# Optimization experiments

Measured on AMD Instinct MI355X. Metric: run time of the kernel, lower is better.

Reference implementation:

```python
import jax, jax.numpy as jnp
import numpy as np

COMMITMENT_COST = 0.25
EPS = 1e-10


def setup_inputs() -> dict:
    key = jax.random.key(0)
    k1, k2 = jax.random.split(key)
    B, C, H, W = 16, 64, 128, 128          # C == embedding_dim
    K, D = 512, 64                          # codebook size, embedding_dim
    inputs = jax.random.normal(k1, (B, C, H, W), dtype=jnp.float32)
    # nn.Embedding init: uniform(-1/K, 1/K)
    embedding = jax.random.uniform(k2, (K, D), dtype=jnp.float32,
                                   minval=-1.0 / K, maxval=1.0 / K)
    return {"inputs": inputs, "embedding": embedding}


def reference(inputs, embedding):
    # NCHW -> NHWC, flatten to tokens [N, D]
    x = jnp.transpose(inputs, (0, 2, 3, 1))
    nhwc_shape = x.shape
    flat = x.reshape(-1, embedding.shape[1])                       # [N, D]

    distances = (jnp.sum(flat * flat, axis=1, keepdims=True)
                 + jnp.sum(embedding * embedding, axis=1)
                 - 2.0 * flat @ embedding.T)
    idx = jnp.argmin(distances, axis=1)                            # [N]

    # one-hot encodings (returned), quantized via direct gather
    encodings = jax.nn.one_hot(idx, embedding.shape[0], dtype=flat.dtype)  # [N, K]
    quantized = embedding[idx].reshape(nhwc_shape)                 # [B,H,W,D]

    e_latent = jnp.mean((jax.lax.stop_gradient(quantized) - x) ** 2)
    q_latent = jnp.mean((quantized - jax.lax.stop_gradient(x)) ** 2)
    loss = q_latent + COMMITMENT_COST * e_latent

    # straight-through estimator
    quantized_st = x + jax.lax.stop_gradient(quantized - x)

    avg_probs = jnp.mean(encodings, axis=0)                        # [K]
    perplexity = jnp.exp(-jnp.sum(avg_probs * jnp.log(avg_probs + EPS)))

    return (loss, jnp.transpose(quantized_st, (0, 3, 1, 2)), perplexity, encodings)
```

## Files before the change

kernel.cpp:

```cpp
#include <hip/hip_runtime.h>
#include <math.h>


#define NTOK    262144
#define KCODES  512
#define DDIM    64
#define CSTRIDE 16384
#define IMG     1048576
#define QOFF    1
#define POFF    16777217
#define EOFF    16777218
#define BK      8192
#define LOSS    8704
#define EBF     12800
#define SUBFLT  32768

typedef short bf16x8 __attribute__((ext_vector_type(8)));
typedef float f32x4  __attribute__((ext_vector_type(4)));

__device__ __forceinline__ unsigned short f2bf(float f) {
    unsigned u = __float_as_uint(f);
    return (unsigned short)((u + 0x7fffu + ((u >> 16) & 1u)) >> 16);
}

__device__ __forceinline__ float np_pairwise_sq64(const float* v) {
    float r[8];
#pragma unroll
    for (int j = 0; j < 8; ++j) r[j] = __fmul_rn(v[j], v[j]);
#pragma unroll
    for (int i = 8; i < 64; i += 8) {
#pragma unroll
        for (int j = 0; j < 8; ++j)
            r[j] = __fadd_rn(r[j], __fmul_rn(v[i + j], v[i + j]));
    }
    float s01 = __fadd_rn(r[0], r[1]);
    float s23 = __fadd_rn(r[2], r[3]);
    float s45 = __fadd_rn(r[4], r[5]);
    float s67 = __fadd_rn(r[6], r[7]);
    return __fadd_rn(__fadd_rn(s01, s23), __fadd_rn(s45, s67));
}

__global__ __launch_bounds__(256) void vq_prep(const float* __restrict__ emb,
                                               float* __restrict__ ws) {
    const int tid = threadIdx.x, blk = blockIdx.x;
    if (blk < 8) {
        unsigned short* ebf = (unsigned short*)(ws + EBF);
#pragma unroll
        for (int ii = 0; ii < 16; ++ii) {
            int t = blk * 4096 + ii * 256 + tid;
            ebf[t] = f2bf(emb[t]);
        }
    } else {
#pragma unroll
        for (int r = 0; r < 2; ++r) {
            const int k = tid * 2 + r;
            const float* e = emb + (size_t)k * DDIM;
            float v[64];
#pragma unroll
            for (int i = 0; i < 64; ++i) v[i] = e[i];
            ws[BK + k] = np_pairwise_sq64(v);
        }
    }
}

__global__ __launch_bounds__(256, 4) void vq_main(const float* __restrict__ in,
                                                  const float* __restrict__ emb,
                                                  float* __restrict__ out,
                                                  float* __restrict__ ws) {
    __shared__ unsigned short xbf[64 * 68];
    __shared__ float          xls[64 * 64];
    __shared__ float          bsh[512];
    __shared__ int            idx_sh[64];
    __shared__ float          red[4];

    const int tid = threadIdx.x, blk = blockIdx.x;
    const int T0 = blk * 64, b = T0 >> 14, hw0 = T0 & 16383;

    const float4* gx = (const float4*)(in + (size_t)b * IMG + hw0);
    float4 g[4];
#pragma unroll
    for (int jj = 0; jj < 4; ++jj) {
        int t = tid + jj * 256;
        g[jj] = gx[(size_t)(t >> 4) * (CSTRIDE / 4) + (t & 15)];
    }
    const float bk0 = ws[BK + tid];
    const float bk1 = ws[BK + 256 + tid];

    f32x4* sub4 = (f32x4*)(out + EOFF + (size_t)blk * SUBFLT);
    const f32x4 z4 = {0.f, 0.f, 0.f, 0.f};
#pragma unroll
    for (int ii = 0; ii < 32; ++ii)
        __builtin_nontemporal_store(z4, sub4 + ii * 256 + tid);

#pragma unroll
    for (int jj = 0; jj < 4; ++jj) {
        int t = tid + jj * 256;
        int c = t >> 4, q4 = (t & 15) * 4;
        *(float4*)(&xls[c * 64 + q4]) = g[jj];
        xbf[(q4 + 0) * 68 + c] = f2bf(g[jj].x);
        xbf[(q4 + 1) * 68 + c] = f2bf(g[jj].y);
        xbf[(q4 + 2) * 68 + c] = f2bf(g[jj].z);
        xbf[(q4 + 3) * 68 + c] = f2bf(g[jj].w);
    }
    bsh[tid]       = bk0;
    bsh[256 + tid] = bk1;
    __syncthreads();

    const int l = tid & 63, w = tid >> 6;
    const int lm = l & 15, lg = l >> 4;

    const bf16x8 a0 = *(const bf16x8*)(xbf + (w * 16 + lm) * 68 + lg * 8);
    const bf16x8 a1 = *(const bf16x8*)(xbf + (w * 16 + lm) * 68 + 32 + lg * 8);

    const unsigned short* ebf = (const unsigned short*)(ws + EBF);
    const unsigned short* ep  = ebf + lm * 64 + lg * 8;

    float dmin[4]; int idx[4];
#pragma unroll
    for (int r = 0; r < 4; ++r) { dmin[r] = 3.402823466e38f; idx[r] = 0; }
    const f32x4 zero = {0.f, 0.f, 0.f, 0.f};

#pragma unroll 4
    for (int nt = 0; nt < 32; ++nt) {
        bf16x8 b0 = *(const bf16x8*)(ep + nt * 1024);
        bf16x8 b1 = *(const bf16x8*)(ep + nt * 1024 + 32);
        f32x4 acc = __builtin_amdgcn_mfma_f32_16x16x32_bf16(a0, b0, zero, 0, 0, 0);
        acc       = __builtin_amdgcn_mfma_f32_16x16x32_bf16(a1, b1, acc,  0, 0, 0);
        const int   code = nt * 16 + lm;
        const float bk   = bsh[code];
#pragma unroll
        for (int r = 0; r < 4; ++r) {
            float s = fmaf(-2.0f, acc[r], bk);
            if (s < dmin[r]) { dmin[r] = s; idx[r] = code; }
        }
    }

#pragma unroll
    for (int m = 1; m < 16; m <<= 1) {
#pragma unroll
        for (int r = 0; r < 4; ++r) {
            float od = __shfl_xor(dmin[r], m, 64);
            int   oi = __shfl_xor(idx[r],  m, 64);
            if (od < dmin[r] || (od == dmin[r] && oi < idx[r])) {
                dmin[r] = od; idx[r] = oi;
            }
        }
    }
    if (lm == 0) {
#pragma unroll
        for (int r = 0; r < 4; ++r) idx_sh[w * 16 + lg * 4 + r] = idx[r];
    }
    __syncthreads();

    const int tl = tid & 63, chh = (tid >> 6) * 16;
    const int id = idx_sh[tl];

    const float4* e4 = (const float4*)(emb + (size_t)id * DDIM + chh);
    float4 ev[4];
#pragma unroll
    for (int k = 0; k < 4; ++k) ev[k] = e4[k];

    float* q = out + QOFF + (size_t)b * IMG + hw0 + tl;
    float lsum = 0.f;
#pragma unroll
    for (int cc = 0; cc < 16; ++cc) {
        float x   = xls[(chh + cc) * 64 + tl];
        float e   = (cc & 2) ? ((cc & 1) ? 0.f : 0.f) : 0.f;
        (void)e;
        float ee  = ((const float*)&ev[cc >> 2])[cc & 3];
        float dqx = __fsub_rn(ee, x);
        lsum = __fadd_rn(lsum, __fmul_rn(dqx, dqx));
        __builtin_nontemporal_store(__fadd_rn(x, dqx),
                                    q + (size_t)(chh + cc) * CSTRIDE);
    }
#pragma unroll
    for (int off = 32; off > 0; off >>= 1) lsum += __shfl_down(lsum, off, 64);
    if ((tid & 63) == 0) red[tid >> 6] = lsum;
    __syncthreads();
    if (tid == 0) ws[LOSS + blk] = red[0] + red[1] + red[2] + red[3];

    if (tid < 64) {
        const int ix = idx_sh[tid];
        f32x4 v = {0.f, 0.f, 0.f, 0.f};
        v[ix & 3] = 1.0f;
        __builtin_nontemporal_store(v, sub4 + tid * 128 + (ix >> 2));
        atomicAdd((int*)ws + ((blk & 15) << 9) + ix, 1);
    }
}

__global__ void vq_final(float* __restrict__ out, const float* __restrict__ ws) {
    __shared__ float sl[512], sp[512];
    int t = threadIdx.x;
    float s = 0.f;
#pragma unroll
    for (int r = 0; r < 8; ++r) s += ws[LOSS + t + 512 * r];
    sl[t] = s;
    int cnt = 0;
#pragma unroll
    for (int r = 0; r < 16; ++r) cnt += ((const int*)ws)[(r << 9) + t];
    float p = (float)cnt * (1.0f / 262144.0f);
    sp[t] = p * logf(p + 1e-10f);
    __syncthreads();
    for (int off = 256; off > 0; off >>= 1) {
        if (t < off) { sl[t] += sl[t + off]; sp[t] += sp[t + off]; }
        __syncthreads();
    }
    if (t == 0) {
        float m = sl[0] * (1.0f / 16777216.0f);
        out[0]    = __fadd_rn(m, __fmul_rn(0.25f, m));
        out[POFF] = expf(-sp[0]);
    }
}

extern "C" void kernel_launch(void* const* d_in, const int* in_sizes, int n_in,
                              void* d_out, int out_size, void* d_ws, size_t ws_size,
                              hipStream_t stream) {
    const float* in  = (const float*)d_in[0];
    const float* emb = (const float*)d_in[1];
    float* out = (float*)d_out;
    float* ws  = (float*)d_ws;

    (void)hipMemsetAsync(d_ws, 0, 16 * 512 * sizeof(int), stream);
    hipLaunchKernelGGL(vq_prep,  dim3(9),    dim3(256), 0, stream, emb, ws);
    hipLaunchKernelGGL(vq_main,  dim3(4096), dim3(256), 0, stream, in, emb, out, ws);
    hipLaunchKernelGGL(vq_final, dim3(1),    dim3(512), 0, stream, out, ws);
}
```

Baseline: 726.5 us.

## Process 256 tokens per block and re-read inputs from global in epilogue

```diff
diff --git a/kernel.cpp b/kernel.cpp
--- a/kernel.cpp
+++ b/kernel.cpp
@@ -13,7 +13,8 @@
 #define BK      8192
 #define LOSS    8704
 #define EBF     12800
-#define SUBFLT  32768
+#define TPB     256
+#define SUBFLT  (TPB * KCODES)
 
 typedef short bf16x8 __attribute__((ext_vector_type(8)));
 typedef float f32x4  __attribute__((ext_vector_type(4)));
@@ -67,111 +68,115 @@
                                                   const float* __restrict__ emb,
                                                   float* __restrict__ out,
                                                   float* __restrict__ ws) {
-    __shared__ unsigned short xbf[64 * 68];
-    __shared__ float          xls[64 * 64];
+    __shared__ unsigned short xbf[TPB * 68];
     __shared__ float          bsh[512];
-    __shared__ int            idx_sh[64];
+    __shared__ int            idx_sh[TPB];
     __shared__ float          red[4];
 
     const int tid = threadIdx.x, blk = blockIdx.x;
-    const int T0 = blk * 64, b = T0 >> 14, hw0 = T0 & 16383;
-
-    const float4* gx = (const float4*)(in + (size_t)b * IMG + hw0);
-    float4 g[4];
-#pragma unroll
-    for (int jj = 0; jj < 4; ++jj) {
-        int t = tid + jj * 256;
-        g[jj] = gx[(size_t)(t >> 4) * (CSTRIDE / 4) + (t & 15)];
-    }
-    const float bk0 = ws[BK + tid];
-    const float bk1 = ws[BK + 256 + tid];
+    const int T0 = blk * TPB, b = T0 >> 14, hw0 = T0 & 16383;
 
     f32x4* sub4 = (f32x4*)(out + EOFF + (size_t)blk * SUBFLT);
     const f32x4 z4 = {0.f, 0.f, 0.f, 0.f};
-#pragma unroll
-    for (int ii = 0; ii < 32; ++ii)
-        __builtin_nontemporal_store(z4, sub4 + ii * 256 + tid);
-
-#pragma unroll
-    for (int jj = 0; jj < 4; ++jj) {
-        int t = tid + jj * 256;
-        int c = t >> 4, q4 = (t & 15) * 4;
-        *(float4*)(&xls[c * 64 + q4]) = g[jj];
-        xbf[(q4 + 0) * 68 + c] = f2bf(g[jj].x);
-        xbf[(q4 + 1) * 68 + c] = f2bf(g[jj].y);
-        xbf[(q4 + 2) * 68 + c] = f2bf(g[jj].z);
-        xbf[(q4 + 3) * 68 + c] = f2bf(g[jj].w);
-    }
-    bsh[tid]       = bk0;
-    bsh[256 + tid] = bk1;
+
+#pragma unroll
+    for (int p = 0; p < 4; ++p) {
+        const float4* gx = (const float4*)(in + (size_t)b * IMG + hw0 + p * 64);
+        float4 g[4];
+#pragma unroll
+        for (int jj = 0; jj < 4; ++jj) {
+            int t = tid + jj * 256;
+            g[jj] = gx[(size_t)(t >> 4) * (CSTRIDE / 4) + (t & 15)];
+        }
+#pragma unroll
+        for (int k = 0; k < 32; ++k)
+            __builtin_nontemporal_store(z4, sub4 + (p * 32 + k) * 256 + tid);
+#pragma unroll
+        for (int jj = 0; jj < 4; ++jj) {
+            int t = tid + jj * 256;
+            int c = t >> 4, q4 = (t & 15) * 4;
+            int row = p * 64 + q4;
+            xbf[(row + 0) * 68 + c] = f2bf(g[jj].x);
+            xbf[(row + 1) * 68 + c] = f2bf(g[jj].y);
+            xbf[(row + 2) * 68 + c] = f2bf(g[jj].z);
+            xbf[(row + 3) * 68 + c] = f2bf(g[jj].w);
+        }
+    }
+    bsh[tid]       = ws[BK + tid];
+    bsh[256 + tid] = ws[BK + 256 + tid];
     __syncthreads();
 
     const int l = tid & 63, w = tid >> 6;
     const int lm = l & 15, lg = l >> 4;
 
-    const bf16x8 a0 = *(const bf16x8*)(xbf + (w * 16 + lm) * 68 + lg * 8);
-    const bf16x8 a1 = *(const bf16x8*)(xbf + (w * 16 + lm) * 68 + 32 + lg * 8);
-
     const unsigned short* ebf = (const unsigned short*)(ws + EBF);
     const unsigned short* ep  = ebf + lm * 64 + lg * 8;
-
-    float dmin[4]; int idx[4];
-#pragma unroll
-    for (int r = 0; r < 4; ++r) { dmin[r] = 3.402823466e38f; idx[r] = 0; }
     const f32x4 zero = {0.f, 0.f, 0.f, 0.f};
 
+#pragma unroll
+    for (int p = 0; p < 4; ++p) {
+        const bf16x8 a0 = *(const bf16x8*)(xbf + (p * 64 + w * 16 + lm) * 68 + lg * 8);
+        const bf16x8 a1 = *(const bf16x8*)(xbf + (p * 64 + w * 16 + lm) * 68 + 32 + lg * 8);
+
+        float dmin[4]; int idx[4];
+#pragma unroll
+        for (int r = 0; r < 4; ++r) { dmin[r] = 3.402823466e38f; idx[r] = 0; }
+
 #pragma unroll 4
-    for (int nt = 0; nt < 32; ++nt) {
-        bf16x8 b0 = *(const bf16x8*)(ep + nt * 1024);
-        bf16x8 b1 = *(const bf16x8*)(ep + nt * 1024 + 32);
-        f32x4 acc = __builtin_amdgcn_mfma_f32_16x16x32_bf16(a0, b0, zero, 0, 0, 0);
-        acc       = __builtin_amdgcn_mfma_f32_16x16x32_bf16(a1, b1, acc,  0, 0, 0);
-        const int   code = nt * 16 + lm;
-        const float bk   = bsh[code];
-#pragma unroll
-        for (int r = 0; r < 4; ++r) {
-            float s = fmaf(-2.0f, acc[r], bk);
-            if (s < dmin[r]) { dmin[r] = s; idx[r] = code; }
-        }
-    }
-
-#pragma unroll
-    for (int m = 1; m < 16; m <<= 1) {
-#pragma unroll
-        for (int r = 0; r < 4; ++r) {
-            float od = __shfl_xor(dmin[r], m, 64);
-            int   oi = __shfl_xor(idx[r],  m, 64);
-            if (od < dmin[r] || (od == dmin[r] && oi < idx[r])) {
-                dmin[r] = od; idx[r] = oi;
+        for (int nt = 0; nt < 32; ++nt) {
+            bf16x8 b0 = *(const bf16x8*)(ep + nt * 1024);
+            bf16x8 b1 = *(const bf16x8*)(ep + nt * 1024 + 32);
+            f32x4 acc = __builtin_amdgcn_mfma_f32_16x16x32_bf16(a0, b0, zero, 0, 0, 0);
+            acc       = __builtin_amdgcn_mfma_f32_16x16x32_bf16(a1, b1, acc,  0, 0, 0);
+            const int   code = nt * 16 + lm;
+            const float bk   = bsh[code];
+#pragma unroll
+            for (int r = 0; r < 4; ++r) {
+                float s = fmaf(-2.0f, acc[r], bk);
+                if (s < dmin[r]) { dmin[r] = s; idx[r] = code; }
             }
         }
-    }
-    if (lm == 0) {
-#pragma unroll
-        for (int r = 0; r < 4; ++r) idx_sh[w * 16 + lg * 4 + r] = idx[r];
+
+#pragma unroll
+        for (int m = 1; m < 16; m <<= 1) {
+#pragma unroll
+            for (int r = 0; r < 4; ++r) {
+                float od = __shfl_xor(dmin[r], m, 64);
+                int   oi = __shfl_xor(idx[r],  m, 64);
+                if (od < dmin[r] || (od == dmin[r] && oi < idx[r])) {
+                    dmin[r] = od; idx[r] = oi;
+                }
+            }
+        }
+        if (lm == 0) {
+#pragma unroll
+            for (int r = 0; r < 4; ++r)
+                idx_sh[p * 64 + w * 16 + lg * 4 + r] = idx[r];
+        }
     }
     __syncthreads();
 
     const int tl = tid & 63, chh = (tid >> 6) * 16;
-    const int id = idx_sh[tl];
-
-    const float4* e4 = (const float4*)(emb + (size_t)id * DDIM + chh);
-    float4 ev[4];
-#pragma unroll
-    for (int k = 0; k < 4; ++k) ev[k] = e4[k];
-
-    float* q = out + QOFF + (size_t)b * IMG + hw0 + tl;
     float lsum = 0.f;
 #pragma unroll
-    for (int cc = 0; cc < 16; ++cc) {
-        float x   = xls[(chh + cc) * 64 + tl];
-        float e   = (cc & 2) ? ((cc & 1) ? 0.f : 0.f) : 0.f;
-        (void)e;
-        float ee  = ((const float*)&ev[cc >> 2])[cc & 3];
-        float dqx = __fsub_rn(ee, x);
-        lsum = __fadd_rn(lsum, __fmul_rn(dqx, dqx));
-        __builtin_nontemporal_store(__fadd_rn(x, dqx),
-                                    q + (size_t)(chh + cc) * CSTRIDE);
+    for (int p = 0; p < 4; ++p) {
+        const int id = idx_sh[p * 64 + tl];
+        const float4* e4 = (const float4*)(emb + (size_t)id * DDIM + chh);
+        float4 ev[4];
+#pragma unroll
+        for (int k = 0; k < 4; ++k) ev[k] = e4[k];
+
+        const float* px = in  + (size_t)b * IMG + hw0 + p * 64 + tl;
+        float*       q  = out + QOFF + (size_t)b * IMG + hw0 + p * 64 + tl;
+#pragma unroll
+        for (int cc = 0; cc < 16; ++cc) {
+            float x   = px[(size_t)(chh + cc) * CSTRIDE];
+            float ee  = ((const float*)&ev[cc >> 2])[cc & 3];
+            float dqx = __fsub_rn(ee, x);
+            lsum = __fadd_rn(lsum, __fmul_rn(dqx, dqx));
+            __builtin_nontemporal_store(__fadd_rn(x, dqx),
+                                        q + (size_t)(chh + cc) * CSTRIDE);
+        }
     }
 #pragma unroll
     for (int off = 32; off > 0; off >>= 1) lsum += __shfl_down(lsum, off, 64);
@@ -179,11 +184,10 @@
     __syncthreads();
     if (tid == 0) ws[LOSS + blk] = red[0] + red[1] + red[2] + red[3];
 
-    if (tid < 64) {
+    {
         const int ix = idx_sh[tid];
-        f32x4 v = {0.f, 0.f, 0.f, 0.f};
-        v[ix & 3] = 1.0f;
-        __builtin_nontemporal_store(v, sub4 + tid * 128 + (ix >> 2));
+        __builtin_nontemporal_store(
+            1.0f, out + EOFF + ((size_t)blk * TPB + tid) * 512 + ix);
         atomicAdd((int*)ws + ((blk & 15) << 9) + ix, 1);
     }
 }
@@ -193,7 +197,7 @@
     int t = threadIdx.x;
     float s = 0.f;
 #pragma unroll
-    for (int r = 0; r < 8; ++r) s += ws[LOSS + t + 512 * r];
+    for (int r = 0; r < 2; ++r) s += ws[LOSS + t + 512 * r];
     sl[t] = s;
     int cnt = 0;
 #pragma unroll
@@ -222,6 +226,6 @@
 
     (void)hipMemsetAsync(d_ws, 0, 16 * 512 * sizeof(int), stream);
     hipLaunchKernelGGL(vq_prep,  dim3(9),    dim3(256), 0, stream, emb, ws);
-    hipLaunchKernelGGL(vq_main,  dim3(4096), dim3(256), 0, stream, in, emb, out, ws);
+    hipLaunchKernelGGL(vq_main,  dim3(1024), dim3(256), 0, stream, in, emb, out, ws);
     hipLaunchKernelGGL(vq_final, dim3(1),    dim3(512), 0, stream, out, ws);
 }
```

Result: slower. 751.5 us (+3.4%).
